# Kernel optimization log

Hardware: AMD Instinct MI355X
Metric: run time of the kernel (lower is better)

The kernel has to match this reference:

```python
import jax, jax.numpy as jnp
import numpy as np

NUM_HEADS = 8
LATENT_FRAME = 4
D_MODEL = 1024
D_FF = 1024  # dim_feedforward == output_dim in the torch module
N_LAYERS = 6
IN_DIM = 128
LN_EPS = 1e-5


def get_slopes(n):
    # standard ALiBi slopes for power-of-two head counts: 2^{-8(i+1)/n}
    return jnp.asarray([2.0 ** (-8.0 * (i + 1) / n) for i in range(n)], jnp.float32)


def alibi_mask(num_heads, T):
    # non-causal ('future') ALiBi: additive bias -slope_h * |i - j|, shape (H, T, T)
    dist = jnp.abs(jnp.arange(T)[:, None] - jnp.arange(T)[None, :]).astype(jnp.float32)
    return -get_slopes(num_heads)[:, None, None] * dist


def layernorm(x, g, b):
    m = jnp.mean(x, axis=-1, keepdims=True)
    v = jnp.mean((x - m) ** 2, axis=-1, keepdims=True)
    return (x - m) * jax.lax.rsqrt(v + LN_EPS) * g + b


def encoder_layer(x, p, mask):
    # torch TransformerEncoderLayer, post-norm, gelu(exact), dropout=0
    B, T, D = x.shape
    H, Dh = NUM_HEADS, D // NUM_HEADS
    qkv = x @ p['in_w'].T + p['in_b']                      # (B,T,3D)
    q, k, v = jnp.split(qkv, 3, axis=-1)
    hsplit = lambda t: t.reshape(B, T, H, Dh).transpose(0, 2, 1, 3)  # (B,H,T,Dh)
    q, k, v = hsplit(q), hsplit(k), hsplit(v)
    scores = jnp.einsum('bhqd,bhkd->bhqk', q, k) / float(np.sqrt(Dh)) + mask[None]
    attn = jax.nn.softmax(scores, axis=-1)
    o = jnp.einsum('bhqk,bhkd->bhqd', attn, v).transpose(0, 2, 1, 3).reshape(B, T, D)
    o = o @ p['out_w'].T + p['out_b']
    x = layernorm(x + o, p['ln1_g'], p['ln1_b'])
    ff = jax.nn.gelu(x @ p['ff1_w'].T + p['ff1_b'], approximate=False) @ p['ff2_w'].T + p['ff2_b']
    return layernorm(x + ff, p['ln2_g'], p['ln2_b'])


def setup_inputs() -> dict:
    key = jax.random.key(0)
    ks = iter(jax.random.split(key, 32))
    s = 0.02
    B, T, F = 8, 2048, IN_DIM
    Fs = F * LATENT_FRAME  # 512
    inp = {
        'x': jax.random.normal(next(ks), (B, T, F), jnp.float32),
        'pre_w': jax.random.normal(next(ks), (D_MODEL, Fs), jnp.float32) * s,
        'pre_b': jnp.zeros((D_MODEL,), jnp.float32),
        'in_w': jax.random.normal(next(ks), (N_LAYERS, 3 * D_MODEL, D_MODEL), jnp.float32) * s,
        'in_b': jnp.zeros((N_LAYERS, 3 * D_MODEL), jnp.float32),
        'out_w': jax.random.normal(next(ks), (N_LAYERS, D_MODEL, D_MODEL), jnp.float32) * s,
        'out_b': jnp.zeros((N_LAYERS, D_MODEL), jnp.float32),
        'ln1_g': jnp.ones((N_LAYERS, D_MODEL), jnp.float32),
        'ln1_b': jnp.zeros((N_LAYERS, D_MODEL), jnp.float32),
        'ff1_w': jax.random.normal(next(ks), (N_LAYERS, D_FF, D_MODEL), jnp.float32) * s,
        'ff1_b': jnp.zeros((N_LAYERS, D_FF), jnp.float32),
        'ff2_w': jax.random.normal(next(ks), (N_LAYERS, D_MODEL, D_FF), jnp.float32) * s,
        'ff2_b': jnp.zeros((N_LAYERS, D_MODEL), jnp.float32),
        'ln2_g': jnp.ones((N_LAYERS, D_MODEL), jnp.float32),
        'ln2_b': jnp.zeros((N_LAYERS, D_MODEL), jnp.float32),
        'post_w': jax.random.normal(next(ks), (D_MODEL, D_MODEL), jnp.float32) * s,
        'post_b': jnp.zeros((D_MODEL,), jnp.float32),
    }
    return inp


def reference(x, pre_w, pre_b, in_w, in_b, out_w, out_b, ln1_g, ln1_b,
              ff1_w, ff1_b, ff2_w, ff2_b, ln2_g, ln2_b, post_w, post_b):
    B, T, F = x.shape
    Tl = T // LATENT_FRAME
    x = x.reshape(B, Tl, F * LATENT_FRAME)
    x = x @ pre_w.T + pre_b                     # (B, Tl, D)
    mask = alibi_mask(NUM_HEADS, Tl)            # (H, Tl, Tl), shared by all batches
    layers = dict(in_w=in_w, in_b=in_b, out_w=out_w, out_b=out_b,
                  ln1_g=ln1_g, ln1_b=ln1_b, ff1_w=ff1_w, ff1_b=ff1_b,
                  ff2_w=ff2_w, ff2_b=ff2_b, ln2_g=ln2_g, ln2_b=ln2_b)
    def step(h, p):
        return encoder_layer(h, p, mask), None
    x, _ = jax.lax.scan(step, x, layers)
    return x @ post_w.T + post_b
```

## Files before the change

### kernel.cpp

```cpp
#include <hip/hip_runtime.h>
#include <hip/hip_bf16.h>

#define B 8
#define TL 512
#define M_ROWS 4096
#define D 1024
#define DFF 1024
#define H 8
#define DH 128
#define NL 6

typedef unsigned short ushort_t;
typedef unsigned int uint_t;
typedef short bf16x8 __attribute__((ext_vector_type(8)));
typedef float f32x4 __attribute__((ext_vector_type(4)));

__device__ __forceinline__ ushort_t f2bf(float f) {
    uint_t u = __float_as_uint(f);
    u += 0x7FFFu + ((u >> 16) & 1u);
    return (ushort_t)(u >> 16);
}
__device__ __forceinline__ float gelu_exact(float x) {
    return 0.5f * x * (1.0f + erff(x * 0.70710678118654752f));
}
__device__ __forceinline__ void gload_lds16(const ushort_t* g, ushort_t* l) {
    __builtin_amdgcn_global_load_lds(
        (const __attribute__((address_space(1))) void*)g,
        (__attribute__((address_space(3))) void*)l, 16, 0, 0);
}

struct CvtArgs {
    const float* s[7];
    ushort_t* d[7];
    int nq[7];
    int bstart[8];
};

__global__ __launch_bounds__(256) void cvt_all(CvtArgs a) {
    const int bid = blockIdx.x;
#pragma unroll
    for (int seg = 0; seg < 7; ++seg) {
        const int b0 = a.bstart[seg], b1 = a.bstart[seg + 1];
        if (bid < b0 || bid >= b1) continue;
        const int stride = (b1 - b0) * 256;
        const float* s = a.s[seg];
        ushort_t* d = a.d[seg];
        const int nq = a.nq[seg];
        for (int i = (bid - b0) * 256 + threadIdx.x; i < nq; i += stride) {
            float4 v0 = *(const float4*)(s + (size_t)i * 8);
            float4 v1 = *(const float4*)(s + (size_t)i * 8 + 4);
            uint4 pk;
            pk.x = (uint_t)f2bf(v0.x) | ((uint_t)f2bf(v0.y) << 16);
            pk.y = (uint_t)f2bf(v0.z) | ((uint_t)f2bf(v0.w) << 16);
            pk.z = (uint_t)f2bf(v1.x) | ((uint_t)f2bf(v1.y) << 16);
            pk.w = (uint_t)f2bf(v1.z) | ((uint_t)f2bf(v1.w) << 16);
            *(uint4*)(d + (size_t)i * 8) = pk;
        }
    }
}

#define LSLOT64(r, c) (((r) * 8 + ((c) ^ ((r) & 7))) * 8)

__global__ __launch_bounds__(256) void gemm_n64(
    const ushort_t* __restrict__ A, const ushort_t* __restrict__ W,
    const float* __restrict__ bias, const float* __restrict__ resid,
    float* __restrict__ Cf, ushort_t* __restrict__ Cb,
    int M, int N, int K, int do_gelu) {
    __shared__ ushort_t As[128 * 64];
    __shared__ ushort_t Bs[64 * 64];

    const int tid = threadIdx.x;
    const int lane = tid & 63;
    const int w = tid >> 6;
    const int wm = (w & 2) * 32;
    const int wn = (w & 1) * 32;
    const int bm = blockIdx.y * 128;
    const int bn = blockIdx.x * 64;

    const ushort_t* gA[4];
    ushort_t* lA[4];
#pragma unroll
    for (int t = 0; t < 4; ++t) {
        int s = tid + t * 256;
        int r = s >> 3, gl = (s & 7) ^ (r & 7);
        gA[t] = A + (size_t)(bm + r) * K + gl * 8;
        lA[t] = &As[s * 8];
    }
    const ushort_t* gB[2];
    ushort_t* lB[2];
#pragma unroll
    for (int t = 0; t < 2; ++t) {
        int s = tid + t * 256;
        int r = s >> 3, gl = (s & 7) ^ (r & 7);
        gB[t] = W + (size_t)(bn + r) * K + gl * 8;
        lB[t] = &Bs[s * 8];
    }

    const int fr = lane & 15;
    const int fq = lane >> 4;
    int aoff[4][2], boff[2][2];
#pragma unroll
    for (int t = 0; t < 4; ++t)
#pragma unroll
        for (int s = 0; s < 2; ++s)
            aoff[t][s] = LSLOT64(wm + t * 16 + fr, s * 4 + fq);
#pragma unroll
    for (int t = 0; t < 2; ++t)
#pragma unroll
        for (int s = 0; s < 2; ++s)
            boff[t][s] = LSLOT64(wn + t * 16 + fr, s * 4 + fq);

    f32x4 acc[4][2];
#pragma unroll
    for (int i = 0; i < 4; ++i)
#pragma unroll
        for (int j = 0; j < 2; ++j) acc[i][j] = (f32x4){0.f, 0.f, 0.f, 0.f};

    for (int k0 = 0; k0 < K; k0 += 64) {
#pragma unroll
        for (int t = 0; t < 4; ++t) gload_lds16(gA[t] + k0, lA[t]);
#pragma unroll
        for (int t = 0; t < 2; ++t) gload_lds16(gB[t] + k0, lB[t]);
        __syncthreads();

#pragma unroll
        for (int s = 0; s < 2; ++s) {
            bf16x8 af[4], bf[2];
#pragma unroll
            for (int t = 0; t < 4; ++t) af[t] = *(const bf16x8*)&As[aoff[t][s]];
#pragma unroll
            for (int t = 0; t < 2; ++t) bf[t] = *(const bf16x8*)&Bs[boff[t][s]];
#pragma unroll
            for (int i = 0; i < 4; ++i)
#pragma unroll
                for (int j = 0; j < 2; ++j)
                    acc[i][j] = __builtin_amdgcn_mfma_f32_16x16x32_bf16(
                        af[i], bf[j], acc[i][j], 0, 0, 0);
        }
        __syncthreads();
    }

#pragma unroll
    for (int tj = 0; tj < 2; ++tj) {
        const int n = bn + wn + tj * 16 + fr;
        const float bv = bias[n];
#pragma unroll
        for (int ti = 0; ti < 4; ++ti) {
            const int m0 = bm + wm + ti * 16 + fq * 4;
            f32x4 a = acc[ti][tj];
#pragma unroll
            for (int r = 0; r < 4; ++r) {
                float v = a[r] + bv;
                if (do_gelu) v = gelu_exact(v);
                const size_t off = (size_t)(m0 + r) * N + n;
                if (resid) v += resid[off];
                if (Cf) Cf[off] = v;
                if (Cb) Cb[off] = f2bf(v);
            }
        }
    }
}

__global__ __launch_bounds__(256) void gemm_qkv(
    const ushort_t* __restrict__ A, const ushort_t* __restrict__ W,
    const float* __restrict__ bias, ushort_t* __restrict__ Qb,
    ushort_t* __restrict__ Kb, ushort_t* __restrict__ Vt, int K) {
    __shared__ ushort_t As[128 * 64];
    __shared__ ushort_t Bs[128 * 64];

    const int tid = threadIdx.x;
    const int lane = tid & 63;
    const int w = tid >> 6;
    const int wm = (w >> 1) * 64;
    const int wn = (w & 1) * 64;
    const int bm = blockIdx.y * 128;
    const int bn = blockIdx.x * 128;

    const ushort_t* gA[4];
    const ushort_t* gB[4];
    ushort_t* lA[4];
    ushort_t* lB[4];
#pragma unroll
    for (int t = 0; t < 4; ++t) {
        int s = tid + t * 256;
        int r = s >> 3, gl = (s & 7) ^ (r & 7);
        gA[t] = A + (size_t)(bm + r) * K + gl * 8;
        gB[t] = W + (size_t)(bn + r) * K + gl * 8;
        lA[t] = &As[s * 8];
        lB[t] = &Bs[s * 8];
    }

    const int fr = lane & 15;
    const int fq = lane >> 4;
    int aoff[4][2], boff[4][2];
#pragma unroll
    for (int t = 0; t < 4; ++t)
#pragma unroll
        for (int s = 0; s < 2; ++s) {
            aoff[t][s] = LSLOT64(wm + t * 16 + fr, s * 4 + fq);
            boff[t][s] = LSLOT64(wn + t * 16 + fr, s * 4 + fq);
        }

    f32x4 acc[4][4];
#pragma unroll
    for (int i = 0; i < 4; ++i)
#pragma unroll
        for (int j = 0; j < 4; ++j) acc[i][j] = (f32x4){0.f, 0.f, 0.f, 0.f};

    for (int k0 = 0; k0 < K; k0 += 64) {
#pragma unroll
        for (int t = 0; t < 4; ++t) gload_lds16(gA[t] + k0, lA[t]);
#pragma unroll
        for (int t = 0; t < 4; ++t) gload_lds16(gB[t] + k0, lB[t]);
        __syncthreads();

#pragma unroll
        for (int s = 0; s < 2; ++s) {
            bf16x8 af[4], bf[4];
#pragma unroll
            for (int t = 0; t < 4; ++t) af[t] = *(const bf16x8*)&As[aoff[t][s]];
#pragma unroll
            for (int t = 0; t < 4; ++t) bf[t] = *(const bf16x8*)&Bs[boff[t][s]];
#pragma unroll
            for (int i = 0; i < 4; ++i)
#pragma unroll
                for (int j = 0; j < 4; ++j)
                    acc[i][j] = __builtin_amdgcn_mfma_f32_16x16x32_bf16(
                        af[i], bf[j], acc[i][j], 0, 0, 0);
        }
        __syncthreads();
    }

    const float qscale = 0.08838834764831845f;
#pragma unroll
    for (int tj = 0; tj < 4; ++tj) {
        const int n = bn + wn + tj * 16 + fr;
        const float bv = bias[n];
#pragma unroll
        for (int ti = 0; ti < 4; ++ti) {
            const int m0 = bm + wm + ti * 16 + fq * 4;
            f32x4 a = acc[ti][tj];
            if (n < D) {
#pragma unroll
                for (int r = 0; r < 4; ++r)
                    Qb[(size_t)(m0 + r) * D + n] = f2bf((a[r] + bv) * qscale);
            } else if (n < 2 * D) {
#pragma unroll
                for (int r = 0; r < 4; ++r)
                    Kb[(size_t)(m0 + r) * D + (n - D)] = f2bf(a[r] + bv);
            } else {
                const int h = (n - 2 * D) >> 7;
                const int dh = (n - 2 * D) & 127;
                const int bb = m0 >> 9;
                const int t = m0 & 511;
                ushort4 pk;
                pk.x = f2bf(a[0] + bv); pk.y = f2bf(a[1] + bv);
                pk.z = f2bf(a[2] + bv); pk.w = f2bf(a[3] + bv);
                *(ushort4*)&Vt[((size_t)(bb * H + h) * DH + dh) * TL + t] = pk;
            }
        }
    }
}

#define LSW16(r, g) ((((r) << 4) + ((g) ^ ((r) & 7))) << 3)
#define LSW8(r, g) ((((r) << 3) + ((g) ^ ((r) & 7))) << 3)

__global__ __launch_bounds__(256, 2) void attn_mfma(
    const ushort_t* __restrict__ Qb, const ushort_t* __restrict__ Kb,
    const ushort_t* __restrict__ Vt, ushort_t* __restrict__ Ab) {
    __shared__ ushort_t Qs[64 * 128];
    __shared__ ushort_t Ks[64 * 128];
    __shared__ ushort_t Vts[128 * 64];
    __shared__ ushort_t Ps[64 * 72];

    const int q0 = blockIdx.x * 64;
    const int bh = blockIdx.y;
    const int b = bh >> 3;
    const int h = bh & 7;
    const int tid = threadIdx.x;
    const int lane = tid & 63;
    const int w = tid >> 6;
    const int fr = lane & 15;
    const int fq = lane >> 4;

    const float slope = exp2f(-(float)(h + 1));

#pragma unroll
    for (int kk = 0; kk < 4; ++kk) {
        int s = tid + kk * 256;
        int r = s >> 4, gp = s & 15, gl = gp ^ (r & 7);
        gload_lds16(Qb + (size_t)(b * TL + q0 + r) * D + h * DH + gl * 8,
                    &Qs[s * 8]);
    }

    f32x4 o8[8];
    float m_i[4], l_i[4];
#pragma unroll
    for (int nt = 0; nt < 8; ++nt) o8[nt] = (f32x4){0.f, 0.f, 0.f, 0.f};
#pragma unroll
    for (int r = 0; r < 4; ++r) { m_i[r] = -1e30f; l_i[r] = 0.f; }

    for (int kt = 0; kt < TL / 64; ++kt) {
        __syncthreads();
#pragma unroll
        for (int kk = 0; kk < 4; ++kk) {
            int s = tid + kk * 256;
            int r = s >> 4, gp = s & 15, gl = gp ^ (r & 7);
            gload_lds16(Kb + (size_t)(b * TL + kt * 64 + r) * D + h * DH + gl * 8,
                        &Ks[s * 8]);
        }
#pragma unroll
        for (int kk = 0; kk < 4; ++kk) {
            int s = tid + kk * 256;
            int r = s >> 3, gp = s & 7, gl = gp ^ (r & 7);
            gload_lds16(Vt + ((size_t)bh * DH + r) * TL + kt * 64 + gl * 8,
                        &Vts[s * 8]);
        }
        __syncthreads();

        f32x4 sacc[4];
#pragma unroll
        for (int jt = 0; jt < 4; ++jt) sacc[jt] = (f32x4){0.f, 0.f, 0.f, 0.f};
#pragma unroll
        for (int s4 = 0; s4 < 4; ++s4) {
            bf16x8 aq = *(const bf16x8*)&Qs[LSW16(w * 16 + fr, s4 * 4 + fq)];
#pragma unroll
            for (int jt = 0; jt < 4; ++jt) {
                bf16x8 kb = *(const bf16x8*)&Ks[LSW16(jt * 16 + fr, s4 * 4 + fq)];
                sacc[jt] = __builtin_amdgcn_mfma_f32_16x16x32_bf16(
                    aq, kb, sacc[jt], 0, 0, 0);
            }
        }

        const int iq = q0 + w * 16 + fq * 4;
        const int jk = kt * 64 + fr;
        float al[4];
#pragma unroll
        for (int r = 0; r < 4; ++r) {
            float sv[4];
#pragma unroll
            for (int jt = 0; jt < 4; ++jt)
                sv[jt] = sacc[jt][r] -
                         slope * fabsf((float)(iq + r - jk - jt * 16));
            float mx = fmaxf(fmaxf(sv[0], sv[1]), fmaxf(sv[2], sv[3]));
            mx = fmaxf(mx, __shfl_xor(mx, 1));
            mx = fmaxf(mx, __shfl_xor(mx, 2));
            mx = fmaxf(mx, __shfl_xor(mx, 4));
            mx = fmaxf(mx, __shfl_xor(mx, 8));
            float mnew = fmaxf(m_i[r], mx);
            al[r] = __expf(m_i[r] - mnew);
            float rs = 0.f;
#pragma unroll
            for (int jt = 0; jt < 4; ++jt) {
                sv[jt] = __expf(sv[jt] - mnew);
                rs += sv[jt];
            }
            rs += __shfl_xor(rs, 1);
            rs += __shfl_xor(rs, 2);
            rs += __shfl_xor(rs, 4);
            rs += __shfl_xor(rs, 8);
            l_i[r] = l_i[r] * al[r] + rs;
            m_i[r] = mnew;
            const int prow = w * 16 + fq * 4 + r;
#pragma unroll
            for (int jt = 0; jt < 4; ++jt)
                Ps[prow * 72 + jt * 16 + fr] = f2bf(sv[jt]);
        }
#pragma unroll
        for (int nt = 0; nt < 8; ++nt)
#pragma unroll
            for (int r = 0; r < 4; ++r) o8[nt][r] *= al[r];

#pragma unroll
        for (int s2 = 0; s2 < 2; ++s2) {
            bf16x8 pa = *(const bf16x8*)&Ps[(w * 16 + fr) * 72 + s2 * 32 + fq * 8];
#pragma unroll
            for (int nt = 0; nt < 8; ++nt) {
                bf16x8 vb = *(const bf16x8*)&Vts[LSW8(nt * 16 + fr, s2 * 4 + fq)];
                o8[nt] = __builtin_amdgcn_mfma_f32_16x16x32_bf16(
                    pa, vb, o8[nt], 0, 0, 0);
            }
        }
    }

#pragma unroll
    for (int r = 0; r < 4; ++r) {
        float inv = 1.f / l_i[r];
        const size_t base = (size_t)(b * TL + q0 + w * 16 + fq * 4 + r) * D + h * DH;
#pragma unroll
        for (int nt = 0; nt < 8; ++nt)
            Ab[base + nt * 16 + fr] = f2bf(o8[nt][r] * inv);
    }
}

__global__ __launch_bounds__(256) void add_ln(const float* __restrict__ Y,
                                              const float* __restrict__ g,
                                              const float* __restrict__ bta,
                                              float* __restrict__ out,
                                              ushort_t* __restrict__ outb) {
    const int row = blockIdx.x * 4 + (threadIdx.x >> 6);
    const int lane = threadIdx.x & 63;
    const size_t rbase = (size_t)row * D;

    float4 v[4];
#pragma unroll
    for (int j = 0; j < 4; ++j)
        v[j] = *(const float4*)(Y + rbase + lane * 4 + j * 256);

    float s = 0.f;
#pragma unroll
    for (int j = 0; j < 4; ++j) s += v[j].x + v[j].y + v[j].z + v[j].w;
#pragma unroll
    for (int off = 32; off; off >>= 1) s += __shfl_xor(s, off);
    const float mean = s * (1.f / (float)D);

    float sq = 0.f;
#pragma unroll
    for (int j = 0; j < 4; ++j) {
        float d0 = v[j].x - mean, d1 = v[j].y - mean;
        float d2 = v[j].z - mean, d3 = v[j].w - mean;
        sq += d0 * d0 + d1 * d1 + d2 * d2 + d3 * d3;
    }
#pragma unroll
    for (int off = 32; off; off >>= 1) sq += __shfl_xor(sq, off);
    const float var = sq * (1.f / (float)D);
    const float inv = rsqrtf(var + 1e-5f);

#pragma unroll
    for (int j = 0; j < 4; ++j) {
        const int col = lane * 4 + j * 256;
        float4 gv = *(const float4*)(g + col);
        float4 bv = *(const float4*)(bta + col);
        float4 o;
        o.x = (v[j].x - mean) * inv * gv.x + bv.x;
        o.y = (v[j].y - mean) * inv * gv.y + bv.y;
        o.z = (v[j].z - mean) * inv * gv.z + bv.z;
        o.w = (v[j].w - mean) * inv * gv.w + bv.w;
        *(float4*)(out + rbase + col) = o;
        ushort4 ob;
        ob.x = f2bf(o.x); ob.y = f2bf(o.y); ob.z = f2bf(o.z); ob.w = f2bf(o.w);
        *(ushort4*)(outb + rbase + col) = ob;
    }
}

extern "C" void kernel_launch(void* const* d_in, const int* in_sizes, int n_in,
                              void* d_out, int out_size, void* d_ws, size_t ws_size,
                              hipStream_t stream) {
    const float* x_in   = (const float*)d_in[0];
    const float* pre_w  = (const float*)d_in[1];
    const float* pre_b  = (const float*)d_in[2];
    const float* in_w   = (const float*)d_in[3];
    const float* in_b   = (const float*)d_in[4];
    const float* out_w  = (const float*)d_in[5];
    const float* out_b  = (const float*)d_in[6];
    const float* ln1_g  = (const float*)d_in[7];
    const float* ln1_b  = (const float*)d_in[8];
    const float* ff1_w  = (const float*)d_in[9];
    const float* ff1_b  = (const float*)d_in[10];
    const float* ff2_w  = (const float*)d_in[11];
    const float* ff2_b  = (const float*)d_in[12];
    const float* ln2_g  = (const float*)d_in[13];
    const float* ln2_b  = (const float*)d_in[14];
    const float* post_w = (const float*)d_in[15];
    const float* post_b = (const float*)d_in[16];

    float* X = (float*)d_ws;
    float* Y = X + (size_t)M_ROWS * D;
    ushort_t* Xb   = (ushort_t*)(Y + (size_t)M_ROWS * D);
    ushort_t* Ab   = Xb + (size_t)M_ROWS * D;
    ushort_t* Qb   = Ab + (size_t)M_ROWS * D;
    ushort_t* Kb   = Qb + (size_t)M_ROWS * D;
    ushort_t* Vt   = Kb + (size_t)M_ROWS * D;
    ushort_t* xinb = Vt + (size_t)M_ROWS * D;
    ushort_t* pwb  = xinb + (size_t)M_ROWS * 512;
    ushort_t* iwb  = pwb + (size_t)D * 512;
    ushort_t* owb  = iwb + (size_t)NL * 3 * D * D;
    ushort_t* f1wb = owb + (size_t)NL * D * D;
    ushort_t* f2wb = f1wb + (size_t)NL * DFF * D;
    ushort_t* powb = f2wb + (size_t)NL * D * DFF;

    const dim3 blk(256);

    CvtArgs ca;
    ca.s[0] = x_in;   ca.d[0] = xinb; ca.nq[0] = (M_ROWS * 512) / 8;
    ca.s[1] = pre_w;  ca.d[1] = pwb;  ca.nq[1] = (D * 512) / 8;
    ca.s[2] = in_w;   ca.d[2] = iwb;  ca.nq[2] = (NL * 3 * D * D) / 8;
    ca.s[3] = out_w;  ca.d[3] = owb;  ca.nq[3] = (NL * D * D) / 8;
    ca.s[4] = ff1_w;  ca.d[4] = f1wb; ca.nq[4] = (NL * DFF * D) / 8;
    ca.s[5] = ff2_w;  ca.d[5] = f2wb; ca.nq[5] = (NL * D * DFF) / 8;
    ca.s[6] = post_w; ca.d[6] = powb; ca.nq[6] = (D * D) / 8;
    {
        long long total = 0;
        for (int i = 0; i < 7; ++i) total += ca.nq[i];
        long long cum = 0;
        ca.bstart[0] = 0;
        for (int i = 0; i < 7; ++i) {
            cum += ca.nq[i];
            ca.bstart[i + 1] = (int)((cum * 4096) / total);
        }
        ca.bstart[7] = 4096;
    }
    cvt_all<<<4096, blk, 0, stream>>>(ca);

    const dim3 gN64(D / 64, M_ROWS / 128);
    const dim3 gQKV(3 * D / 128, M_ROWS / 128);

    gemm_n64<<<gN64, blk, 0, stream>>>(xinb, pwb, pre_b, nullptr, X, Xb,
                                       M_ROWS, D, 512, 0);

    for (int l = 0; l < NL; ++l) {
        gemm_qkv<<<gQKV, blk, 0, stream>>>(Xb, iwb + (size_t)l * 3 * D * D,
                                           in_b + (size_t)l * 3 * D,
                                           Qb, Kb, Vt, D);
        attn_mfma<<<dim3(TL / 64, B * H), blk, 0, stream>>>(Qb, Kb, Vt, Ab);
        gemm_n64<<<gN64, blk, 0, stream>>>(Ab, owb + (size_t)l * D * D,
                                           out_b + (size_t)l * D, X, Y, nullptr,
                                           M_ROWS, D, D, 0);
        add_ln<<<dim3(M_ROWS / 4), blk, 0, stream>>>(Y, ln1_g + (size_t)l * D,
                                                     ln1_b + (size_t)l * D, X, Xb);
        gemm_n64<<<gN64, blk, 0, stream>>>(Xb, f1wb + (size_t)l * DFF * D,
                                           ff1_b + (size_t)l * DFF, nullptr,
                                           nullptr, Ab, M_ROWS, DFF, D, 1);
        gemm_n64<<<gN64, blk, 0, stream>>>(Ab, f2wb + (size_t)l * D * DFF,
                                           ff2_b + (size_t)l * D, X, Y, nullptr,
                                           M_ROWS, D, DFF, 0);
        add_ln<<<dim3(M_ROWS / 4), blk, 0, stream>>>(Y, ln2_g + (size_t)l * D,
                                                     ln2_b + (size_t)l * D, X, Xb);
    }

    gemm_n64<<<gN64, blk, 0, stream>>>(Xb, powb, post_b, nullptr,
                                       (float*)d_out, nullptr, M_ROWS, D, D, 0);
}
```

Before: 1.219 ms.

## Double-buffer GEMM LDS tiles, move residual add into LayerNorm, narrow cvt loads

Both GEMM kernels now use two LDS buffers. The next K-tile's global-to-LDS loads are issued before computing the current tile, and an explicit waitcnt-plus-barrier drains between stages. The residual add leaves the GEMM epilogue and moves into add_ln, which now reads X and Y separately. The conversion kernel processes 4 floats per thread instead of 8. Double buffering doubles LDS use, which can lower occupancy, and the cvt change means more, smaller memory ops.

New measurement: 1.289 ms. +5.7%, slower.

```diff
diff --git a/kernel.cpp b/kernel.cpp
--- a/kernel.cpp
+++ b/kernel.cpp
@@ -28,6 +28,11 @@
         (const __attribute__((address_space(1))) void*)g,
         (__attribute__((address_space(3))) void*)l, 16, 0, 0);
 }
+__device__ __forceinline__ void gsync_drain() {
+    asm volatile("s_waitcnt vmcnt(0) lgkmcnt(0)" ::: "memory");
+    __builtin_amdgcn_sched_barrier(0);
+    __builtin_amdgcn_s_barrier();
+}
 
 struct CvtArgs {
     const float* s[7];
@@ -47,14 +52,10 @@
         ushort_t* d = a.d[seg];
         const int nq = a.nq[seg];
         for (int i = (bid - b0) * 256 + threadIdx.x; i < nq; i += stride) {
-            float4 v0 = *(const float4*)(s + (size_t)i * 8);
-            float4 v1 = *(const float4*)(s + (size_t)i * 8 + 4);
-            uint4 pk;
-            pk.x = (uint_t)f2bf(v0.x) | ((uint_t)f2bf(v0.y) << 16);
-            pk.y = (uint_t)f2bf(v0.z) | ((uint_t)f2bf(v0.w) << 16);
-            pk.z = (uint_t)f2bf(v1.x) | ((uint_t)f2bf(v1.y) << 16);
-            pk.w = (uint_t)f2bf(v1.z) | ((uint_t)f2bf(v1.w) << 16);
-            *(uint4*)(d + (size_t)i * 8) = pk;
+            float4 v = *(const float4*)(s + (size_t)i * 4);
+            ushort4 o;
+            o.x = f2bf(v.x); o.y = f2bf(v.y); o.z = f2bf(v.z); o.w = f2bf(v.w);
+            *(ushort4*)(d + (size_t)i * 4) = o;
         }
     }
 }
@@ -63,11 +64,10 @@
 
 __global__ __launch_bounds__(256) void gemm_n64(
     const ushort_t* __restrict__ A, const ushort_t* __restrict__ W,
-    const float* __restrict__ bias, const float* __restrict__ resid,
-    float* __restrict__ Cf, ushort_t* __restrict__ Cb,
-    int M, int N, int K, int do_gelu) {
-    __shared__ ushort_t As[128 * 64];
-    __shared__ ushort_t Bs[64 * 64];
+    const float* __restrict__ bias, float* __restrict__ Cf,
+    ushort_t* __restrict__ Cb, int M, int N, int K, int do_gelu) {
+    __shared__ ushort_t As[2][128 * 64];
+    __shared__ ushort_t Bs[2][64 * 64];
 
     const int tid = threadIdx.x;
     const int lane = tid & 63;
@@ -78,22 +78,22 @@
     const int bn = blockIdx.x * 64;
 
     const ushort_t* gA[4];
-    ushort_t* lA[4];
+    int sA[4];
 #pragma unroll
     for (int t = 0; t < 4; ++t) {
         int s = tid + t * 256;
         int r = s >> 3, gl = (s & 7) ^ (r & 7);
         gA[t] = A + (size_t)(bm + r) * K + gl * 8;
-        lA[t] = &As[s * 8];
+        sA[t] = s * 8;
     }
     const ushort_t* gB[2];
-    ushort_t* lB[2];
+    int sB[2];
 #pragma unroll
     for (int t = 0; t < 2; ++t) {
         int s = tid + t * 256;
         int r = s >> 3, gl = (s & 7) ^ (r & 7);
         gB[t] = W + (size_t)(bn + r) * K + gl * 8;
-        lB[t] = &Bs[s * 8];
+        sB[t] = s * 8;
     }
 
     const int fr = lane & 15;
@@ -116,28 +116,40 @@
 #pragma unroll
         for (int j = 0; j < 2; ++j) acc[i][j] = (f32x4){0.f, 0.f, 0.f, 0.f};
 
-    for (int k0 = 0; k0 < K; k0 += 64) {
-#pragma unroll
-        for (int t = 0; t < 4; ++t) gload_lds16(gA[t] + k0, lA[t]);
-#pragma unroll
-        for (int t = 0; t < 2; ++t) gload_lds16(gB[t] + k0, lB[t]);
-        __syncthreads();
-
+    auto stage = [&](int buf, int k0) {
+#pragma unroll
+        for (int t = 0; t < 4; ++t) gload_lds16(gA[t] + k0, &As[buf][sA[t]]);
+#pragma unroll
+        for (int t = 0; t < 2; ++t) gload_lds16(gB[t] + k0, &Bs[buf][sB[t]]);
+    };
+    auto comp = [&](int buf) {
 #pragma unroll
         for (int s = 0; s < 2; ++s) {
-            bf16x8 af[4], bf[2];
-#pragma unroll
-            for (int t = 0; t < 4; ++t) af[t] = *(const bf16x8*)&As[aoff[t][s]];
-#pragma unroll
-            for (int t = 0; t < 2; ++t) bf[t] = *(const bf16x8*)&Bs[boff[t][s]];
+            bf16x8 af[4], bfv[2];
+#pragma unroll
+            for (int t = 0; t < 4; ++t)
+                af[t] = *(const bf16x8*)&As[buf][aoff[t][s]];
+#pragma unroll
+            for (int t = 0; t < 2; ++t)
+                bfv[t] = *(const bf16x8*)&Bs[buf][boff[t][s]];
 #pragma unroll
             for (int i = 0; i < 4; ++i)
 #pragma unroll
                 for (int j = 0; j < 2; ++j)
                     acc[i][j] = __builtin_amdgcn_mfma_f32_16x16x32_bf16(
-                        af[i], bf[j], acc[i][j], 0, 0, 0);
-        }
-        __syncthreads();
+                        af[i], bfv[j], acc[i][j], 0, 0, 0);
+        }
+    };
+
+    stage(0, 0);
+    gsync_drain();
+    for (int k0 = 0; k0 < K; k0 += 128) {
+        stage(1, k0 + 64);
+        comp(0);
+        gsync_drain();
+        if (k0 + 128 < K) stage(0, k0 + 128);
+        comp(1);
+        gsync_drain();
     }
 
 #pragma unroll
@@ -153,7 +165,6 @@
                 float v = a[r] + bv;
                 if (do_gelu) v = gelu_exact(v);
                 const size_t off = (size_t)(m0 + r) * N + n;
-                if (resid) v += resid[off];
                 if (Cf) Cf[off] = v;
                 if (Cb) Cb[off] = f2bf(v);
             }
@@ -165,8 +176,8 @@
     const ushort_t* __restrict__ A, const ushort_t* __restrict__ W,
     const float* __restrict__ bias, ushort_t* __restrict__ Qb,
     ushort_t* __restrict__ Kb, ushort_t* __restrict__ Vt, int K) {
-    __shared__ ushort_t As[128 * 64];
-    __shared__ ushort_t Bs[128 * 64];
+    __shared__ ushort_t As[2][128 * 64];
+    __shared__ ushort_t Bs[2][128 * 64];
 
     const int tid = threadIdx.x;
     const int lane = tid & 63;
@@ -178,16 +189,14 @@
 
     const ushort_t* gA[4];
     const ushort_t* gB[4];
-    ushort_t* lA[4];
-    ushort_t* lB[4];
+    int sAB[4];
 #pragma unroll
     for (int t = 0; t < 4; ++t) {
         int s = tid + t * 256;
         int r = s >> 3, gl = (s & 7) ^ (r & 7);
         gA[t] = A + (size_t)(bm + r) * K + gl * 8;
         gB[t] = W + (size_t)(bn + r) * K + gl * 8;
-        lA[t] = &As[s * 8];
-        lB[t] = &Bs[s * 8];
+        sAB[t] = s * 8;
     }
 
     const int fr = lane & 15;
@@ -207,28 +216,40 @@
 #pragma unroll
         for (int j = 0; j < 4; ++j) acc[i][j] = (f32x4){0.f, 0.f, 0.f, 0.f};
 
-    for (int k0 = 0; k0 < K; k0 += 64) {
-#pragma unroll
-        for (int t = 0; t < 4; ++t) gload_lds16(gA[t] + k0, lA[t]);
-#pragma unroll
-        for (int t = 0; t < 4; ++t) gload_lds16(gB[t] + k0, lB[t]);
-        __syncthreads();
-
+    auto stage = [&](int buf, int k0) {
+#pragma unroll
+        for (int t = 0; t < 4; ++t) gload_lds16(gA[t] + k0, &As[buf][sAB[t]]);
+#pragma unroll
+        for (int t = 0; t < 4; ++t) gload_lds16(gB[t] + k0, &Bs[buf][sAB[t]]);
+    };
+    auto comp = [&](int buf) {
 #pragma unroll
         for (int s = 0; s < 2; ++s) {
-            bf16x8 af[4], bf[4];
-#pragma unroll
-            for (int t = 0; t < 4; ++t) af[t] = *(const bf16x8*)&As[aoff[t][s]];
-#pragma unroll
-            for (int t = 0; t < 4; ++t) bf[t] = *(const bf16x8*)&Bs[boff[t][s]];
+            bf16x8 af[4], bfv[4];
+#pragma unroll
+            for (int t = 0; t < 4; ++t)
+                af[t] = *(const bf16x8*)&As[buf][aoff[t][s]];
+#pragma unroll
+            for (int t = 0; t < 4; ++t)
+                bfv[t] = *(const bf16x8*)&Bs[buf][boff[t][s]];
 #pragma unroll
             for (int i = 0; i < 4; ++i)
 #pragma unroll
                 for (int j = 0; j < 4; ++j)
                     acc[i][j] = __builtin_amdgcn_mfma_f32_16x16x32_bf16(
-                        af[i], bf[j], acc[i][j], 0, 0, 0);
-        }
-        __syncthreads();
+                        af[i], bfv[j], acc[i][j], 0, 0, 0);
+        }
+    };
+
+    stage(0, 0);
+    gsync_drain();
+    for (int k0 = 0; k0 < K; k0 += 128) {
+        stage(1, k0 + 64);
+        comp(0);
+        gsync_drain();
+        if (k0 + 128 < K) stage(0, k0 + 128);
+        comp(1);
+        gsync_drain();
     }
 
     const float qscale = 0.08838834764831845f;
@@ -393,7 +414,8 @@
     }
 }
 
-__global__ __launch_bounds__(256) void add_ln(const float* __restrict__ Y,
+__global__ __launch_bounds__(256) void add_ln(const float* __restrict__ x,
+                                              const float* __restrict__ y,
                                               const float* __restrict__ g,
                                               const float* __restrict__ bta,
                                               float* __restrict__ out,
@@ -404,8 +426,12 @@
 
     float4 v[4];
 #pragma unroll
-    for (int j = 0; j < 4; ++j)
-        v[j] = *(const float4*)(Y + rbase + lane * 4 + j * 256);
+    for (int j = 0; j < 4; ++j) {
+        float4 xv = *(const float4*)(x + rbase + lane * 4 + j * 256);
+        float4 yv = *(const float4*)(y + rbase + lane * 4 + j * 256);
+        v[j].x = xv.x + yv.x; v[j].y = xv.y + yv.y;
+        v[j].z = xv.z + yv.z; v[j].w = xv.w + yv.w;
+    }
 
     float s = 0.f;
 #pragma unroll
@@ -482,13 +508,13 @@
     const dim3 blk(256);
 
     CvtArgs ca;
-    ca.s[0] = x_in;   ca.d[0] = xinb; ca.nq[0] = (M_ROWS * 512) / 8;
-    ca.s[1] = pre_w;  ca.d[1] = pwb;  ca.nq[1] = (D * 512) / 8;
-    ca.s[2] = in_w;   ca.d[2] = iwb;  ca.nq[2] = (NL * 3 * D * D) / 8;
-    ca.s[3] = out_w;  ca.d[3] = owb;  ca.nq[3] = (NL * D * D) / 8;
-    ca.s[4] = ff1_w;  ca.d[4] = f1wb; ca.nq[4] = (NL * DFF * D) / 8;
-    ca.s[5] = ff2_w;  ca.d[5] = f2wb; ca.nq[5] = (NL * D * DFF) / 8;
-    ca.s[6] = post_w; ca.d[6] = powb; ca.nq[6] = (D * D) / 8;
+    ca.s[0] = x_in;   ca.d[0] = xinb; ca.nq[0] = (M_ROWS * 512) / 4;
+    ca.s[1] = pre_w;  ca.d[1] = pwb;  ca.nq[1] = (D * 512) / 4;
+    ca.s[2] = in_w;   ca.d[2] = iwb;  ca.nq[2] = (NL * 3 * D * D) / 4;
+    ca.s[3] = out_w;  ca.d[3] = owb;  ca.nq[3] = (NL * D * D) / 4;
+    ca.s[4] = ff1_w;  ca.d[4] = f1wb; ca.nq[4] = (NL * DFF * D) / 4;
+    ca.s[5] = ff2_w;  ca.d[5] = f2wb; ca.nq[5] = (NL * D * DFF) / 4;
+    ca.s[6] = post_w; ca.d[6] = powb; ca.nq[6] = (D * D) / 4;
     {
         long long total = 0;
         for (int i = 0; i < 7; ++i) total += ca.nq[i];
@@ -505,7 +531,7 @@
     const dim3 gN64(D / 64, M_ROWS / 128);
     const dim3 gQKV(3 * D / 128, M_ROWS / 128);
 
-    gemm_n64<<<gN64, blk, 0, stream>>>(xinb, pwb, pre_b, nullptr, X, Xb,
+    gemm_n64<<<gN64, blk, 0, stream>>>(xinb, pwb, pre_b, X, Xb,
                                        M_ROWS, D, 512, 0);
 
     for (int l = 0; l < NL; ++l) {
@@ -514,20 +540,20 @@
                                            Qb, Kb, Vt, D);
         attn_mfma<<<dim3(TL / 64, B * H), blk, 0, stream>>>(Qb, Kb, Vt, Ab);
         gemm_n64<<<gN64, blk, 0, stream>>>(Ab, owb + (size_t)l * D * D,
-                                           out_b + (size_t)l * D, X, Y, nullptr,
+                                           out_b + (size_t)l * D, Y, nullptr,
                                            M_ROWS, D, D, 0);
-        add_ln<<<dim3(M_ROWS / 4), blk, 0, stream>>>(Y, ln1_g + (size_t)l * D,
+        add_ln<<<dim3(M_ROWS / 4), blk, 0, stream>>>(X, Y, ln1_g + (size_t)l * D,
                                                      ln1_b + (size_t)l * D, X, Xb);
         gemm_n64<<<gN64, blk, 0, stream>>>(Xb, f1wb + (size_t)l * DFF * D,
-                                           ff1_b + (size_t)l * DFF, nullptr,
-                                           nullptr, Ab, M_ROWS, DFF, D, 1);
+                                           ff1_b + (size_t)l * DFF, nullptr, Ab,
+                                           M_ROWS, DFF, D, 1);
         gemm_n64<<<gN64, blk, 0, stream>>>(Ab, f2wb + (size_t)l * D * DFF,
-                                           ff2_b + (size_t)l * D, X, Y, nullptr,
+                                           ff2_b + (size_t)l * D, Y, nullptr,
                                            M_ROWS, D, DFF, 0);
-        add_ln<<<dim3(M_ROWS / 4), blk, 0, stream>>>(Y, ln2_g + (size_t)l * D,
+        add_ln<<<dim3(M_ROWS / 4), blk, 0, stream>>>(X, Y, ln2_g + (size_t)l * D,
                                                      ln2_b + (size_t)l * D, X, Xb);
     }
 
-    gemm_n64<<<gN64, blk, 0, stream>>>(Xb, powb, post_b, nullptr,
-                                       (float*)d_out, nullptr, M_ROWS, D, D, 0);
-}
+    gemm_n64<<<gN64, blk, 0, stream>>>(Xb, powb, post_b, (float*)d_out, nullptr,
+                                       M_ROWS, D, D, 0);
+}
```
